# Kernel tuning notes

Measured on AMD Instinct MI355X. Metric: run time of the kernel, lower is better.

The kernel has to match this reference:

```python
import math
import jax, jax.numpy as jnp
import numpy as np

DIM = 256; DEPTH = 5; FANOUT = 10; VOCAB = 257
B = 16; T = 2048
NEXP = 8; HID = 512; TOPK = 2; TEMP = 1.0; HEADS = 2
CAPACITY = math.ceil(B * TOPK / NEXP * 1.1)  # capacity-based dispatch, =5
LAYER_SIZES = [FANOUT ** l for l in range(DEPTH)]  # [1,10,100,1000,10000]


def setup_inputs() -> dict:
    key = jax.random.key(0)
    ks = iter(jax.random.split(key, 64))
    def p(shape, scale=0.02):
        return jax.random.normal(next(ks), shape, jnp.float32) * scale
    inp = {
        'tokens': jax.random.randint(next(ks), (B, T), 0, VOCAB),
        'embed': p((VOCAB, DIM)),
        'pin_w': p((DIM, DIM)), 'pin_b': jnp.zeros(DIM, jnp.float32),
        'pch_w': p((DIM, DIM)), 'pch_b': jnp.zeros(DIM, jnp.float32),
        'depth_bias': p((DEPTH, DIM)),
        'q_w': p((DIM, DIM)), 'q_b': jnp.zeros(DIM, jnp.float32),
        'k_w': p((DIM, DIM)), 'k_b': jnp.zeros(DIM, jnp.float32),
        'v_w': p((DIM, DIM)), 'v_b': jnp.zeros(DIM, jnp.float32),
        'o_w': p((DIM, DIM)), 'o_b': jnp.zeros(DIM, jnp.float32),
        'level_gate': jnp.zeros(DEPTH, jnp.float32),
        'depth_gate': jnp.zeros((DEPTH, DIM), jnp.float32),
        'in_proj_w': p((DIM, 3 * DIM)), 'in_proj_b': jnp.zeros(3 * DIM, jnp.float32),
        'out_proj_w': p((DIM, DIM)), 'out_proj_b': jnp.zeros(DIM, jnp.float32),
        'ln_g': jnp.ones(DIM, jnp.float32), 'ln_b': jnp.zeros(DIM, jnp.float32),
        'ic_gate': jnp.zeros(1, jnp.float32),
        'gate_w': p((DIM, NEXP)), 'gate_b': jnp.zeros(NEXP, jnp.float32),
        'ew1': p((NEXP, DIM, HID)), 'eb1': jnp.zeros((NEXP, HID), jnp.float32),
        'ew2': p((NEXP, HID, DIM)), 'eb2': jnp.zeros((NEXP, DIM), jnp.float32),
        'hw1': p((DIM, DIM)), 'hb1': jnp.zeros(DIM, jnp.float32),
        'hw2': p((DIM, VOCAB)), 'hb2': jnp.zeros(VOCAB, jnp.float32),
    }
    return inp


def _fractal(context, pin_w, pin_b, pch_w, pch_b, depth_bias, q_w, q_b, k_w, k_b,
             v_w, v_b, o_w, o_b, level_gate, depth_gate,
             in_proj_w, in_proj_b, out_proj_w, out_proj_b, ln_g, ln_b, ic_gate):
    Bc = context.shape[0]
    base = context @ pin_w + pin_b                       # [B,D]
    y_next = None
    level_means = [None] * DEPTH
    inv_sqrt_d = 1.0 / math.sqrt(DIM)
    for l in reversed(range(DEPTH)):
        n = LAYER_SIZES[l]
        if l == DEPTH - 1:
            child_agg = jnp.zeros((Bc, n, DIM), context.dtype)
        else:
            yg = y_next.reshape(Bc, n, FANOUT, DIM)      # children grouped per parent
            q = (base + depth_bias[l]) @ q_w + q_b       # [B,D], shared across nodes
            k = yg @ k_w + k_b
            v = yg @ v_w + v_b
            att = jax.nn.softmax(jnp.einsum('bd,bnfd->bnf', q, k) * inv_sqrt_d, axis=-1)
            child_agg = jax.nn.sigmoid(depth_gate[l]) * jnp.einsum('bnf,bnfd->bnd', att, v)
        gate = jax.nn.sigmoid(level_gate[l])
        upd = (base[:, None, :] + depth_bias[l][None, None, :] + child_agg @ pch_w + pch_b) * gate
        y = jax.nn.relu(upd) @ o_w + o_b                 # [B,n,D]
        level_means[l] = y.mean(axis=1)
        y_next = y
    root = y_next[:, 0, :]                               # n==1 at level 0
    # interconnect: MHA over per-level means [B,DEPTH,D]
    z = jnp.stack(level_means, axis=1)
    qkv = z @ in_proj_w + in_proj_b
    qh, kh, vh = jnp.split(qkv, 3, axis=-1)
    hd = DIM // HEADS
    def to_heads(t):
        return t.reshape(Bc, DEPTH, HEADS, hd).transpose(0, 2, 1, 3)
    qh, kh, vh = to_heads(qh), to_heads(kh), to_heads(vh)
    aw = jax.nn.softmax(jnp.einsum('bhqd,bhkd->bhqk', qh, kh) / math.sqrt(hd), axis=-1)
    z2 = jnp.einsum('bhqk,bhkd->bhqd', aw, vh).transpose(0, 2, 1, 3).reshape(Bc, DEPTH, DIM)
    z2 = z2 @ out_proj_w + out_proj_b
    zs = z + z2
    mu = zs.mean(-1, keepdims=True)
    var = ((zs - mu) ** 2).mean(-1, keepdims=True)
    zn = (zs - mu) / jnp.sqrt(var + 1e-5) * ln_g + ln_b
    return root + jax.nn.sigmoid(ic_gate) * zn[:, 0, :]


def _moe(ctx, gate_w, gate_b, ew1, eb1, ew2, eb2):
    scaled = (ctx @ gate_w + gate_b) / TEMP
    top_vals, top_idx = jax.lax.top_k(scaled, TOPK)      # [B,K]
    gs = jax.nn.softmax(top_vals, axis=-1)               # [B,K], strictly > 0
    out = jnp.zeros_like(ctx)
    for e in range(NEXP):                                # fixed small expert loop
        sflat = jnp.where(top_idx == e, gs, -1.0).reshape(-1)   # [B*K]
        vals, pos = jax.lax.top_k(sflat, CAPACITY)       # capacity-limited dispatch
        w = jnp.where(vals > 0.0, vals, 0.0)             # drop unassigned/overflow
        tok = pos // TOPK
        xin = ctx[tok]                                   # [cap,D]
        eo = jax.nn.relu(xin @ ew1[e] + eb1[e]) @ ew2[e] + eb2[e]
        out = out.at[tok].add(eo * w[:, None])
    return out


def reference(tokens, embed, pin_w, pin_b, pch_w, pch_b, depth_bias,
              q_w, q_b, k_w, k_b, v_w, v_b, o_w, o_b, level_gate, depth_gate,
              in_proj_w, in_proj_b, out_proj_w, out_proj_b, ln_g, ln_b, ic_gate,
              gate_w, gate_b, ew1, eb1, ew2, eb2, hw1, hb1, hw2, hb2):
    x = embed[tokens]                                    # [B,T,D]
    context = x.mean(axis=1)                             # [B,D]
    root = _fractal(context, pin_w, pin_b, pch_w, pch_b, depth_bias, q_w, q_b,
                    k_w, k_b, v_w, v_b, o_w, o_b, level_gate, depth_gate,
                    in_proj_w, in_proj_b, out_proj_w, out_proj_b, ln_g, ln_b, ic_gate)
    root = root + _moe(root, gate_w, gate_b, ew1, eb1, ew2, eb2)
    h = x + root[:, None, :]                             # per-token logits from context + token emb
    logits = jax.nn.relu(h @ hw1 + hb1) @ hw2 + hb2      # [B,T,V]
    return logits
```

## Files before the change

kernel.cpp:

```cpp
#include <hip/hip_runtime.h>
#include <hip/hip_bf16.h>
#include <math.h>

#define DIM    256
#define DEPTH  5
#define FANOUT 10
#define VOCAB  257
#define BB     16
#define TT     2048
#define NEXP   8
#define HID    512
#define TOPK   2
#define CAP    5
#define TSTR   260

__device__ __forceinline__ float sigm(float x) { return 1.f / (1.f + expf(-x)); }

__device__ __forceinline__ void mv8x2(const float* sv, const float* __restrict__ W,
                                      int kseg, int cq, float red[16][DIM]) {
  const float* Wp = W + (size_t)kseg * 16 * DIM + cq * 4;
  float4 acc = {0.f, 0.f, 0.f, 0.f};
#pragma unroll 1
  for (int h = 0; h < 2; ++h) {
    float4 wv[8];
#pragma unroll
    for (int i = 0; i < 8; ++i)
      wv[i] = *(const float4*)(Wp + (size_t)(h * 8 + i) * DIM);
#pragma unroll
    for (int i = 0; i < 8; ++i) {
      float s = sv[kseg * 16 + h * 8 + i];
      acc.x = fmaf(s, wv[i].x, acc.x);
      acc.y = fmaf(s, wv[i].y, acc.y);
      acc.z = fmaf(s, wv[i].z, acc.z);
      acc.w = fmaf(s, wv[i].w, acc.w);
    }
    __builtin_amdgcn_sched_barrier(0);
  }
  *(float4*)&red[kseg][cq * 4] = acc;
}

__device__ __forceinline__ float sum16(const float red[16][DIM], int d) {
  float s = 0.f;
#pragma unroll
  for (int g = 0; g < 16; ++g) s += red[g][d];
  return s;
}

__global__ void __launch_bounds__(1024) k_fractal(
    const int* __restrict__ tokens, const float* __restrict__ embed,
    const float* __restrict__ pin_w, const float* __restrict__ pin_b,
    const float* __restrict__ pch_w, const float* __restrict__ pch_b,
    const float* __restrict__ depth_bias,
    const float* __restrict__ v_w, const float* __restrict__ v_b,
    const float* __restrict__ o_w, const float* __restrict__ o_b,
    const float* __restrict__ level_gate, const float* __restrict__ depth_gate,
    const float* __restrict__ in_proj_w, const float* __restrict__ in_proj_b,
    const float* __restrict__ out_proj_w, const float* __restrict__ out_proj_b,
    const float* __restrict__ ln_g, const float* __restrict__ ln_b,
    const float* __restrict__ ic_gate,
    float* __restrict__ rootA) {
  int b = blockIdx.x;
  int tid = threadIdx.x;
  int d = tid & 255;
  int ks = tid >> 8;
  int k0 = ks * 64;
  int kseg = tid >> 6;
  int cq = tid & 63;
  __shared__ int cnt[VOCAB];
  __shared__ float sv[DIM];
  __shared__ float basev[DIM];
  __shared__ float ym[DEPTH][DIM];
  __shared__ float q0v[DIM], kh[DEPTH][DIM], vh[DEPTH][DIM];
  __shared__ float red11[4][11][DIM];
  __shared__ float zsv[DIM];
  __shared__ float aw[16];
  __shared__ float redl[8];
  float (*red16)[DIM] = reinterpret_cast<float(*)[DIM]>(&red11[0][0][0]);

  for (int i = tid; i < VOCAB; i += 1024) cnt[i] = 0;
  __syncthreads();
  for (int t = tid; t < TT; t += 1024) atomicAdd(&cnt[tokens[b * TT + t]], 1);
  __syncthreads();
  {
    const float* Ep = embed + (size_t)kseg * 16 * DIM + cq * 4;
    float4 acc = {0.f, 0.f, 0.f, 0.f};
#pragma unroll 1
    for (int h = 0; h < 2; ++h) {
      float4 ev[8];
#pragma unroll
      for (int i = 0; i < 8; ++i)
        ev[i] = *(const float4*)(Ep + (size_t)(h * 8 + i) * DIM);
#pragma unroll
      for (int i = 0; i < 8; ++i) {
        float cv = (float)cnt[kseg * 16 + h * 8 + i];
        acc.x = fmaf(cv, ev[i].x, acc.x);
        acc.y = fmaf(cv, ev[i].y, acc.y);
        acc.z = fmaf(cv, ev[i].z, acc.z);
        acc.w = fmaf(cv, ev[i].w, acc.w);
      }
      __builtin_amdgcn_sched_barrier(0);
    }
    *(float4*)&red16[kseg][cq * 4] = acc;
  }
  __syncthreads();
  if (ks == 0) {
    float s = sum16(red16, d);
    s = fmaf((float)cnt[256], embed[(size_t)256 * DIM + d], s);
    sv[d] = s * (1.0f / (float)TT);
  }
  __syncthreads();

  mv8x2(sv, pin_w, kseg, cq, red16);
  __syncthreads();
  if (ks == 0) {
    float base = sum16(red16, d) + pin_b[d];
    basev[d] = base;
    float u = (base + depth_bias[4 * DIM + d] + pch_b[d]) * sigm(level_gate[4]);
    sv[d] = fmaxf(u, 0.f);
  }
  __syncthreads();
  mv8x2(sv, o_w, kseg, cq, red16);
  __syncthreads();
  if (ks == 0) {
    float y = sum16(red16, d) + o_b[d];
    ym[4][d] = y;
    sv[d] = y;
  }
  __syncthreads();
  for (int l = 3; l >= 0; --l) {
    mv8x2(sv, v_w, kseg, cq, red16);
    __syncthreads();
    if (ks == 0) {
      float vv = sum16(red16, d) + v_b[d];
      sv[d] = sigm(depth_gate[l * DIM + d]) * vv;
    }
    __syncthreads();
    mv8x2(sv, pch_w, kseg, cq, red16);
    __syncthreads();
    if (ks == 0) {
      float t = sum16(red16, d) + pch_b[d];
      float u = (basev[d] + depth_bias[l * DIM + d] + t) * sigm(level_gate[l]);
      sv[d] = fmaxf(u, 0.f);
    }
    __syncthreads();
    mv8x2(sv, o_w, kseg, cq, red16);
    __syncthreads();
    if (ks == 0) {
      float y = sum16(red16, d) + o_b[d];
      ym[l][d] = y;
      sv[d] = y;
    }
    __syncthreads();
  }
  {
    float aq = 0.f;
    float ak0 = 0.f, ak1 = 0.f, ak2 = 0.f, ak3 = 0.f, ak4 = 0.f;
    float av0 = 0.f, av1 = 0.f, av2 = 0.f, av3 = 0.f, av4 = 0.f;
#pragma unroll
    for (int h = 0; h < 8; ++h) {
      int kb = k0 + h * 8;
      float wq[8], wk[8], wv8[8];
#pragma unroll
      for (int i = 0; i < 8; ++i) {
        const float* wrow = in_proj_w + (size_t)(kb + i) * 768;
        wq[i] = wrow[d]; wk[i] = wrow[256 + d]; wv8[i] = wrow[512 + d];
      }
#pragma unroll
      for (int i = 0; i < 8; ++i) {
        float z0 = ym[0][kb + i];
        aq  = fmaf(z0, wq[i], aq);
        ak0 = fmaf(z0, wk[i], ak0);
        av0 = fmaf(z0, wv8[i], av0);
        float z1 = ym[1][kb + i];
        ak1 = fmaf(z1, wk[i], ak1);
        av1 = fmaf(z1, wv8[i], av1);
        float z2 = ym[2][kb + i];
        ak2 = fmaf(z2, wk[i], ak2);
        av2 = fmaf(z2, wv8[i], av2);
        float z3 = ym[3][kb + i];
        ak3 = fmaf(z3, wk[i], ak3);
        av3 = fmaf(z3, wv8[i], av3);
        float z4 = ym[4][kb + i];
        ak4 = fmaf(z4, wk[i], ak4);
        av4 = fmaf(z4, wv8[i], av4);
      }
    }
    red11[ks][0][d] = ak0; red11[ks][1][d] = ak1; red11[ks][2][d] = ak2;
    red11[ks][3][d] = ak3; red11[ks][4][d] = ak4;
    red11[ks][5][d] = av0; red11[ks][6][d] = av1; red11[ks][7][d] = av2;
    red11[ks][8][d] = av3; red11[ks][9][d] = av4;
    red11[ks][10][d] = aq;
  }
  __syncthreads();
  for (int idx = tid; idx < 11 * DIM; idx += 1024) {
    int c = idx >> 8, dd = idx & 255;
    float sum = red11[0][c][dd] + red11[1][c][dd] + red11[2][c][dd] + red11[3][c][dd];
    if (c < 5)       kh[c][dd]     = sum + in_proj_b[256 + dd];
    else if (c < 10) vh[c - 5][dd] = sum + in_proj_b[512 + dd];
    else             q0v[dd]       = sum + in_proj_b[dd];
  }
  __syncthreads();
  {
    int wid = tid >> 6;
    if (wid < 10) {
      int h = wid / 5, l = wid - h * 5;
      int lane = tid & 63;
      float s = q0v[h * 128 + lane] * kh[l][h * 128 + lane];
      s = fmaf(q0v[h * 128 + 64 + lane], kh[l][h * 128 + 64 + lane], s);
      for (int o = 32; o > 0; o >>= 1) s += __shfl_down(s, o, 64);
      if (lane == 0) aw[wid] = s * 0.08838834764831845f;
    }
  }
  __syncthreads();
  if (tid < 2) {
    float m = aw[tid * 5];
    for (int l = 1; l < 5; ++l) m = fmaxf(m, aw[tid * 5 + l]);
    float e[5], ssum = 0.f;
    for (int l = 0; l < 5; ++l) { e[l] = expf(aw[tid * 5 + l] - m); ssum += e[l]; }
    for (int l = 0; l < 5; ++l) aw[tid * 5 + l] = e[l] / ssum;
  }
  __syncthreads();
  if (ks == 0) {
    int h = d >> 7;
    float z2 = 0.f;
    for (int l = 0; l < 5; ++l) z2 = fmaf(aw[h * 5 + l], vh[l][d], z2);
    sv[d] = z2;
  }
  __syncthreads();
  mv8x2(sv, out_proj_w, kseg, cq, red16);
  __syncthreads();
  if (ks == 0) {
    float z2p = sum16(red16, d) + out_proj_b[d];
    zsv[d] = ym[0][d] + z2p;
  }
  __syncthreads();
  float zs = 0.f, df = 0.f, mu = 0.f;
  if (tid < 256) {
    zs = zsv[tid];
    float v = zs;
    for (int o = 32; o > 0; o >>= 1) v += __shfl_down(v, o, 64);
    if ((tid & 63) == 0) redl[tid >> 6] = v;
  }
  __syncthreads();
  if (tid < 256) {
    mu = (redl[0] + redl[1] + redl[2] + redl[3]) * (1.f / 256.f);
    df = zs - mu;
  }
  __syncthreads();
  if (tid < 256) {
    float v = df * df;
    for (int o = 32; o > 0; o >>= 1) v += __shfl_down(v, o, 64);
    if ((tid & 63) == 0) redl[tid >> 6] = v;
  }
  __syncthreads();
  if (tid < 256) {
    float var = (redl[0] + redl[1] + redl[2] + redl[3]) * (1.f / 256.f);
    float zn = df / sqrtf(var + 1e-5f) * ln_g[tid] + ln_b[tid];
    rootA[b * DIM + tid] = ym[0][tid] + sigm(ic_gate[0]) * zn;
  }
}

__global__ void __launch_bounds__(1024) k_gate(const float* __restrict__ rootA,
                                               const float* __restrict__ gate_w,
                                               const float* __restrict__ gate_b,
                                               int* __restrict__ etok,
                                               float* __restrict__ ewt,
                                               float* __restrict__ root2) {
  __shared__ float red[BB * NEXP][9];
  __shared__ float sc[BB * NEXP];
  __shared__ float gs[BB * TOPK];
  __shared__ int gidx[BB * TOPK];
  int tid = threadIdx.x;
  int be = tid >> 3, ks = tid & 7;
  int b = be >> 3, e = be & 7;
  {
    float acc = 0.f;
#pragma unroll 8
    for (int i = 0; i < 32; ++i) {
      int k = ks * 32 + i;
      acc = fmaf(rootA[b * DIM + k], gate_w[k * NEXP + e], acc);
    }
    red[be][ks] = acc;
  }
  for (int i = tid; i < BB * DIM; i += 1024) root2[i] = rootA[i];
  __syncthreads();
  if (tid < BB * NEXP) {
    float s = gate_b[tid & 7];
#pragma unroll
    for (int g = 0; g < 8; ++g) s += red[tid][g];
    sc[tid] = s;
  }
  __syncthreads();
  if (tid < BB) {
    int bb = tid;
    int i0 = 0; float v0 = sc[bb * 8 + 0];
    for (int ee = 1; ee < 8; ++ee) { float v = sc[bb * 8 + ee]; if (v > v0) { v0 = v; i0 = ee; } }
    int i1 = -1; float v1 = -1e30f;
    for (int ee = 0; ee < 8; ++ee) {
      if (ee == i0) continue;
      float v = sc[bb * 8 + ee];
      if (v > v1) { v1 = v; i1 = ee; }
    }
    float e1 = expf(v1 - v0);
    float s = 1.f + e1;
    gs[bb * 2 + 0] = 1.f / s;  gidx[bb * 2 + 0] = i0;
    gs[bb * 2 + 1] = e1 / s;   gidx[bb * 2 + 1] = i1;
  }
  __syncthreads();
  if (tid < NEXP) {
    int ee = tid;
    unsigned used = 0u;
    for (int s = 0; s < CAP; ++s) {
      int bi = 0; float bv = -1e30f;
      for (int i = 0; i < 32; ++i) {
        if (used & (1u << i)) continue;
        float v = (gidx[i] == ee) ? gs[i] : -1.0f;
        if (v > bv) { bv = v; bi = i; }
      }
      used |= (1u << bi);
      etok[ee * CAP + s] = bi >> 1;
      ewt[ee * CAP + s] = bv > 0.f ? bv : 0.f;
    }
  }
}

__global__ void __launch_bounds__(256) k_expert1(
    const float* __restrict__ rootA,
    const float* __restrict__ ew1, const float* __restrict__ eb1,
    const int* __restrict__ etok,
    float* __restrict__ hid_ws) {
  int bx = blockIdx.x;
  int e = bx >> 3, jt = bx & 7, j0 = jt * 64;
  int tid = threadIdx.x, w = tid >> 6, lane = tid & 63;
  __shared__ float xin[CAP][DIM];
  __shared__ float red[CAP][4][64];
  __shared__ int stok[CAP];
  if (tid < CAP) stok[tid] = etok[e * CAP + tid];
  __syncthreads();
  for (int idx = tid; idx < CAP * DIM; idx += 256) {
    int s = idx >> 8, k = idx & 255;
    xin[s][k] = rootA[stok[s] * DIM + k];
  }
  __syncthreads();
  float a0 = 0.f, a1 = 0.f, a2 = 0.f, a3 = 0.f, a4 = 0.f;
  const float* W = ew1 + (size_t)e * DIM * HID + j0 + lane;
  int kbase = w * 64;
#pragma unroll
  for (int h = 0; h < 8; ++h) {
    float wv[8];
#pragma unroll
    for (int i = 0; i < 8; ++i) wv[i] = W[(size_t)(kbase + h * 8 + i) * HID];
#pragma unroll
    for (int i = 0; i < 8; ++i) {
      int k = kbase + h * 8 + i;
      a0 = fmaf(xin[0][k], wv[i], a0);
      a1 = fmaf(xin[1][k], wv[i], a1);
      a2 = fmaf(xin[2][k], wv[i], a2);
      a3 = fmaf(xin[3][k], wv[i], a3);
      a4 = fmaf(xin[4][k], wv[i], a4);
    }
  }
  red[0][w][lane] = a0; red[1][w][lane] = a1; red[2][w][lane] = a2;
  red[3][w][lane] = a3; red[4][w][lane] = a4;
  __syncthreads();
  for (int idx = tid; idx < CAP * 64; idx += 256) {
    int s = idx >> 6, j = idx & 63;
    float sum = red[s][0][j] + red[s][1][j] + red[s][2][j] + red[s][3][j]
              + eb1[e * HID + j0 + j];
    hid_ws[((size_t)(e * CAP + s)) * HID + j0 + j] = fmaxf(sum, 0.f);
  }
}

__global__ void __launch_bounds__(256) k_expert2(
    const float* __restrict__ hid_ws,
    const float* __restrict__ ew2, const float* __restrict__ eb2,
    const float* __restrict__ ewt, const int* __restrict__ etok,
    float* __restrict__ root2) {
  int bx = blockIdx.x;
  int e = bx >> 3, dt = bx & 7, d0 = dt * 32;
  int tid = threadIdx.x, seg = tid >> 5, c = tid & 31;
  __shared__ float hv[CAP][HID];
  __shared__ float red[CAP][8][32];
  for (int idx = tid; idx < CAP * HID; idx += 256) {
    int s = idx >> 9, k = idx & 511;
    hv[s][k] = hid_ws[((size_t)(e * CAP + s)) * HID + k];
  }
  __syncthreads();
  float a0 = 0.f, a1 = 0.f, a2 = 0.f, a3 = 0.f, a4 = 0.f;
  const float* W = ew2 + (size_t)e * HID * DIM + d0 + c;
  int kbase = seg * 64;
#pragma unroll
  for (int h = 0; h < 8; ++h) {
    float wv[8];
#pragma unroll
    for (int i = 0; i < 8; ++i) wv[i] = W[(size_t)(kbase + h * 8 + i) * DIM];
#pragma unroll
    for (int i = 0; i < 8; ++i) {
      int k = kbase + h * 8 + i;
      a0 = fmaf(hv[0][k], wv[i], a0);
      a1 = fmaf(hv[1][k], wv[i], a1);
      a2 = fmaf(hv[2][k], wv[i], a2);
      a3 = fmaf(hv[3][k], wv[i], a3);
      a4 = fmaf(hv[4][k], wv[i], a4);
    }
  }
  red[0][seg][c] = a0; red[1][seg][c] = a1; red[2][seg][c] = a2;
  red[3][seg][c] = a3; red[4][seg][c] = a4;
  __syncthreads();
  if (tid < CAP * 32) {
    int s = tid >> 5, cc = tid & 31;
    float sum = 0.f;
#pragma unroll
    for (int g = 0; g < 8; ++g) sum += red[s][g][cc];
    sum += eb2[e * DIM + d0 + cc];
    float w = ewt[e * CAP + s];
    if (w > 0.f)
      atomicAdd(&root2[etok[e * CAP + s] * DIM + d0 + cc], sum * w);
  }
}

__global__ void __launch_bounds__(256) k_table(
    const float* __restrict__ embed, const float* __restrict__ root2,
    const float* __restrict__ hw1, const float* __restrict__ hb1,
    const float* __restrict__ hw2, const float* __restrict__ hb2,
    float* __restrict__ table) {
  int tok = blockIdx.x, r0 = blockIdx.y * 4;
  int c = threadIdx.x;
  __shared__ float hrow[4][DIM];
  __shared__ float hid[4][DIM];
  __shared__ float tailred[4][17];
  {
    float ev = embed[(size_t)tok * DIM + c];
#pragma unroll
    for (int j = 0; j < 4; ++j) hrow[j][c] = ev + root2[(size_t)(r0 + j) * DIM + c];
  }
  __syncthreads();
  {
    float a0 = hb1[c], a1 = a0, a2 = a0, a3 = a0;
    for (int kb = 0; kb < DIM; kb += 8) {
      float wv[8];
#pragma unroll
      for (int i = 0; i < 8; ++i) wv[i] = hw1[(size_t)(kb + i) * DIM + c];
#pragma unroll
      for (int i = 0; i < 8; ++i) {
        int k = kb + i;
        a0 = fmaf(hrow[0][k], wv[i], a0);
        a1 = fmaf(hrow[1][k], wv[i], a1);
        a2 = fmaf(hrow[2][k], wv[i], a2);
        a3 = fmaf(hrow[3][k], wv[i], a3);
      }
    }
    hid[0][c] = fmaxf(a0, 0.f); hid[1][c] = fmaxf(a1, 0.f);
    hid[2][c] = fmaxf(a2, 0.f); hid[3][c] = fmaxf(a3, 0.f);
  }
  __syncthreads();
  {
    float a0 = hb2[c], a1 = a0, a2 = a0, a3 = a0;
    for (int kb = 0; kb < DIM; kb += 8) {
      float wv[8];
#pragma unroll
      for (int i = 0; i < 8; ++i) wv[i] = hw2[(size_t)(kb + i) * VOCAB + c];
#pragma unroll
      for (int i = 0; i < 8; ++i) {
        int k = kb + i;
        a0 = fmaf(hid[0][k], wv[i], a0);
        a1 = fmaf(hid[1][k], wv[i], a1);
        a2 = fmaf(hid[2][k], wv[i], a2);
        a3 = fmaf(hid[3][k], wv[i], a3);
      }
    }
    table[((size_t)((r0 + 0) * VOCAB + tok)) * TSTR + c] = a0;
    table[((size_t)((r0 + 1) * VOCAB + tok)) * TSTR + c] = a1;
    table[((size_t)((r0 + 2) * VOCAB + tok)) * TSTR + c] = a2;
    table[((size_t)((r0 + 3) * VOCAB + tok)) * TSTR + c] = a3;
  }
  if (c < 64) {
    int r = c >> 4, seg = c & 15;
    float sum = 0.f;
#pragma unroll 4
    for (int i = 0; i < 16; ++i) {
      int k = seg * 16 + i;
      sum = fmaf(hid[r][k], hw2[(size_t)k * VOCAB + 256], sum);
    }
    tailred[r][seg] = sum;
  }
  __syncthreads();
  if (c < 4) {
    float a = hb2[256];
#pragma unroll
    for (int s = 0; s < 16; ++s) a += tailred[c][s];
    table[((size_t)((r0 + c) * VOCAB + tok)) * TSTR + 256] = a;
  }
}

__global__ void __launch_bounds__(1024) k_scatter(const int* __restrict__ tokens,
                                                  const float* __restrict__ table,
                                                  float* __restrict__ out) {
  int f = blockIdx.x * 1024 + threadIdx.x;
  int row = (int)((unsigned)f / 257u);
  int c = f - row * 257;
  int b = row >> 11;
  int tok = tokens[row];
  out[f] = table[((size_t)(b * VOCAB + tok)) * TSTR + c];
}

extern "C" void kernel_launch(void* const* d_in, const int* in_sizes, int n_in,
                              void* d_out, int out_size, void* d_ws, size_t ws_size,
                              hipStream_t stream) {
  (void)in_sizes; (void)n_in; (void)out_size; (void)ws_size;
  const int*   tokens     = (const int*)d_in[0];
  const float* embed      = (const float*)d_in[1];
  const float* pin_w      = (const float*)d_in[2];
  const float* pin_b      = (const float*)d_in[3];
  const float* pch_w      = (const float*)d_in[4];
  const float* pch_b      = (const float*)d_in[5];
  const float* depth_bias = (const float*)d_in[6];
  const float* v_w        = (const float*)d_in[11];
  const float* v_b        = (const float*)d_in[12];
  const float* o_w        = (const float*)d_in[13];
  const float* o_b        = (const float*)d_in[14];
  const float* level_gate = (const float*)d_in[15];
  const float* depth_gate = (const float*)d_in[16];
  const float* in_proj_w  = (const float*)d_in[17];
  const float* in_proj_b  = (const float*)d_in[18];
  const float* out_proj_w = (const float*)d_in[19];
  const float* out_proj_b = (const float*)d_in[20];
  const float* ln_g       = (const float*)d_in[21];
  const float* ln_b       = (const float*)d_in[22];
  const float* ic_gate    = (const float*)d_in[23];
  const float* gate_w     = (const float*)d_in[24];
  const float* gate_b     = (const float*)d_in[25];
  const float* ew1        = (const float*)d_in[26];
  const float* eb1        = (const float*)d_in[27];
  const float* ew2        = (const float*)d_in[28];
  const float* eb2        = (const float*)d_in[29];
  const float* hw1        = (const float*)d_in[30];
  const float* hb1        = (const float*)d_in[31];
  const float* hw2        = (const float*)d_in[32];
  const float* hb2        = (const float*)d_in[33];
  float* out = (float*)d_out;

  float* ws      = (float*)d_ws;
  float* rootA   = ws + 4096;
  float* root2   = ws + 8192;
  int*   etok    = (int*)(ws + 22528);
  float* ewt     = ws + 22576;
  float* table   = ws + 22656;
  float* hid_ws  = table;

  k_fractal<<<BB, 1024, 0, stream>>>(tokens, embed, pin_w, pin_b, pch_w, pch_b,
                                     depth_bias, v_w, v_b, o_w, o_b, level_gate,
                                     depth_gate, in_proj_w, in_proj_b, out_proj_w,
                                     out_proj_b, ln_g, ln_b, ic_gate, rootA);
  k_gate<<<1, 1024, 0, stream>>>(rootA, gate_w, gate_b, etok, ewt, root2);
  k_expert1<<<NEXP * 8, 256, 0, stream>>>(rootA, ew1, eb1, etok, hid_ws);
  k_expert2<<<NEXP * 8, 256, 0, stream>>>(hid_ws, ew2, eb2, ewt, etok, root2);
  k_table<<<dim3(VOCAB, 4), 256, 0, stream>>>(embed, root2, hw1, hb1, hw2, hb2, table);
  k_scatter<<<(BB * TT * VOCAB) / 1024, 1024, 0, stream>>>(tokens, table, out);
}
```

Before: 264.5 us.

## Fuse gating into expert kernel and scatter logits directly via token buckets

The separate gate kernel is removed: each expert1 block recomputes the gate scores, top-2 selection and capacity assignment redundantly, and root2 is written by the fractal kernel. The fractal kernel also builds per-batch bucket lists of token positions grouped by vocab id. The table kernel then writes each computed logit row straight to every output position holding that token, which eliminates the intermediate table and the separate scatter kernel. Write coalescing now depends on the token distribution, and every expert block repeats the gating work.

Measured after the change: 253.2 us. 1.04x faster.

```diff
diff --git a/kernel.cpp b/kernel.cpp
--- a/kernel.cpp
+++ b/kernel.cpp
@@ -12,7 +12,6 @@
 #define HID    512
 #define TOPK   2
 #define CAP    5
-#define TSTR   260
 
 __device__ __forceinline__ float sigm(float x) { return 1.f / (1.f + expf(-x)); }
 
@@ -58,7 +57,8 @@
     const float* __restrict__ out_proj_w, const float* __restrict__ out_proj_b,
     const float* __restrict__ ln_g, const float* __restrict__ ln_b,
     const float* __restrict__ ic_gate,
-    float* __restrict__ rootA) {
+    float* __restrict__ rootA, float* __restrict__ root2,
+    int* __restrict__ bidx, int* __restrict__ boff) {
   int b = blockIdx.x;
   int tid = threadIdx.x;
   int d = tid & 255;
@@ -75,6 +75,8 @@
   __shared__ float zsv[DIM];
   __shared__ float aw[16];
   __shared__ float redl[8];
+  __shared__ int offb[VOCAB + 1];
+  __shared__ int woff[VOCAB];
   float (*red16)[DIM] = reinterpret_cast<float(*)[DIM]>(&red11[0][0][0]);
 
   for (int i = tid; i < VOCAB; i += 1024) cnt[i] = 0;
@@ -256,38 +258,59 @@
   if (tid < 256) {
     float var = (redl[0] + redl[1] + redl[2] + redl[3]) * (1.f / 256.f);
     float zn = df / sqrtf(var + 1e-5f) * ln_g[tid] + ln_b[tid];
-    rootA[b * DIM + tid] = ym[0][tid] + sigm(ic_gate[0]) * zn;
-  }
-}
-
-__global__ void __launch_bounds__(1024) k_gate(const float* __restrict__ rootA,
-                                               const float* __restrict__ gate_w,
-                                               const float* __restrict__ gate_b,
-                                               int* __restrict__ etok,
-                                               float* __restrict__ ewt,
-                                               float* __restrict__ root2) {
-  __shared__ float red[BB * NEXP][9];
+    float r = ym[0][tid] + sigm(ic_gate[0]) * zn;
+    rootA[b * DIM + tid] = r;
+    root2[b * DIM + tid] = r;
+  }
+  __syncthreads();
+  if (tid == 0) {
+    int a = 0;
+    for (int v = 0; v < VOCAB; ++v) { offb[v] = a; a += cnt[v]; }
+    offb[VOCAB] = a;
+  }
+  __syncthreads();
+  if (tid <= VOCAB) boff[b * (VOCAB + 1) + tid] = offb[tid];
+  if (tid < VOCAB) woff[tid] = offb[tid];
+  __syncthreads();
+  for (int t = tid; t < TT; t += 1024) {
+    int tok = tokens[b * TT + t];
+    int p = atomicAdd(&woff[tok], 1);
+    bidx[b * TT + p] = t;
+  }
+}
+
+__global__ void __launch_bounds__(256) k_expert1(
+    const float* __restrict__ rootA,
+    const float* __restrict__ gate_w, const float* __restrict__ gate_b,
+    const float* __restrict__ ew1, const float* __restrict__ eb1,
+    int* __restrict__ etok, float* __restrict__ ewt,
+    float* __restrict__ hid_ws) {
+  int bx = blockIdx.x;
+  int e = bx >> 3, jt = bx & 7, j0 = jt * 64;
+  int tid = threadIdx.x, w = tid >> 6, lane = tid & 63;
+  __shared__ float xin[CAP][DIM];
+  __shared__ float red[CAP][4][64];
   __shared__ float sc[BB * NEXP];
   __shared__ float gs[BB * TOPK];
   __shared__ int gidx[BB * TOPK];
-  int tid = threadIdx.x;
-  int be = tid >> 3, ks = tid & 7;
-  int b = be >> 3, e = be & 7;
-  {
-    float acc = 0.f;
+  __shared__ int stok[CAP];
+  __shared__ float swt[CAP];
+  if (tid < BB * NEXP) {
+    int b = tid >> 3, ep = tid & 7;
+    float chunk[8];
+#pragma unroll
+    for (int g = 0; g < 8; ++g) {
+      float acc = 0.f;
 #pragma unroll 8
-    for (int i = 0; i < 32; ++i) {
-      int k = ks * 32 + i;
-      acc = fmaf(rootA[b * DIM + k], gate_w[k * NEXP + e], acc);
-    }
-    red[be][ks] = acc;
-  }
-  for (int i = tid; i < BB * DIM; i += 1024) root2[i] = rootA[i];
-  __syncthreads();
-  if (tid < BB * NEXP) {
-    float s = gate_b[tid & 7];
-#pragma unroll
-    for (int g = 0; g < 8; ++g) s += red[tid][g];
+      for (int i = 0; i < 32; ++i) {
+        int k = g * 32 + i;
+        acc = fmaf(rootA[b * DIM + k], gate_w[k * NEXP + ep], acc);
+      }
+      chunk[g] = acc;
+    }
+    float s = gate_b[ep];
+#pragma unroll
+    for (int g = 0; g < 8; ++g) s += chunk[g];
     sc[tid] = s;
   }
   __syncthreads();
@@ -301,42 +324,31 @@
       float v = sc[bb * 8 + ee];
       if (v > v1) { v1 = v; i1 = ee; }
     }
-    float e1 = expf(v1 - v0);
-    float s = 1.f + e1;
+    float e1v = expf(v1 - v0);
+    float s = 1.f + e1v;
     gs[bb * 2 + 0] = 1.f / s;  gidx[bb * 2 + 0] = i0;
-    gs[bb * 2 + 1] = e1 / s;   gidx[bb * 2 + 1] = i1;
-  }
-  __syncthreads();
-  if (tid < NEXP) {
-    int ee = tid;
+    gs[bb * 2 + 1] = e1v / s;  gidx[bb * 2 + 1] = i1;
+  }
+  __syncthreads();
+  if (tid == 0) {
     unsigned used = 0u;
     for (int s = 0; s < CAP; ++s) {
       int bi = 0; float bv = -1e30f;
       for (int i = 0; i < 32; ++i) {
         if (used & (1u << i)) continue;
-        float v = (gidx[i] == ee) ? gs[i] : -1.0f;
+        float v = (gidx[i] == e) ? gs[i] : -1.0f;
         if (v > bv) { bv = v; bi = i; }
       }
       used |= (1u << bi);
-      etok[ee * CAP + s] = bi >> 1;
-      ewt[ee * CAP + s] = bv > 0.f ? bv : 0.f;
-    }
-  }
-}
-
-__global__ void __launch_bounds__(256) k_expert1(
-    const float* __restrict__ rootA,
-    const float* __restrict__ ew1, const float* __restrict__ eb1,
-    const int* __restrict__ etok,
-    float* __restrict__ hid_ws) {
-  int bx = blockIdx.x;
-  int e = bx >> 3, jt = bx & 7, j0 = jt * 64;
-  int tid = threadIdx.x, w = tid >> 6, lane = tid & 63;
-  __shared__ float xin[CAP][DIM];
-  __shared__ float red[CAP][4][64];
-  __shared__ int stok[CAP];
-  if (tid < CAP) stok[tid] = etok[e * CAP + tid];
-  __syncthreads();
+      stok[s] = bi >> 1;
+      swt[s] = bv > 0.f ? bv : 0.f;
+    }
+  }
+  __syncthreads();
+  if (jt == 0 && tid < CAP) {
+    etok[e * CAP + tid] = stok[tid];
+    ewt[e * CAP + tid] = swt[tid];
+  }
   for (int idx = tid; idx < CAP * DIM; idx += 256) {
     int s = idx >> 8, k = idx & 255;
     xin[s][k] = rootA[stok[s] * DIM + k];
@@ -419,16 +431,18 @@
   }
 }
 
-__global__ void __launch_bounds__(256) k_table(
+__global__ void __launch_bounds__(256) k_logits(
     const float* __restrict__ embed, const float* __restrict__ root2,
     const float* __restrict__ hw1, const float* __restrict__ hb1,
     const float* __restrict__ hw2, const float* __restrict__ hb2,
-    float* __restrict__ table) {
+    const int* __restrict__ bidx, const int* __restrict__ boff,
+    float* __restrict__ out) {
   int tok = blockIdx.x, r0 = blockIdx.y * 4;
   int c = threadIdx.x;
   __shared__ float hrow[4][DIM];
   __shared__ float hid[4][DIM];
   __shared__ float tailred[4][17];
+  __shared__ float tailv[4];
   {
     float ev = embed[(size_t)tok * DIM + c];
 #pragma unroll
@@ -454,8 +468,9 @@
     hid[2][c] = fmaxf(a2, 0.f); hid[3][c] = fmaxf(a3, 0.f);
   }
   __syncthreads();
+  float a0, a1, a2, a3;
   {
-    float a0 = hb2[c], a1 = a0, a2 = a0, a3 = a0;
+    a0 = hb2[c]; a1 = a0; a2 = a0; a3 = a0;
     for (int kb = 0; kb < DIM; kb += 8) {
       float wv[8];
 #pragma unroll
@@ -469,10 +484,6 @@
         a3 = fmaf(hid[3][k], wv[i], a3);
       }
     }
-    table[((size_t)((r0 + 0) * VOCAB + tok)) * TSTR + c] = a0;
-    table[((size_t)((r0 + 1) * VOCAB + tok)) * TSTR + c] = a1;
-    table[((size_t)((r0 + 2) * VOCAB + tok)) * TSTR + c] = a2;
-    table[((size_t)((r0 + 3) * VOCAB + tok)) * TSTR + c] = a3;
   }
   if (c < 64) {
     int r = c >> 4, seg = c & 15;
@@ -489,19 +500,23 @@
     float a = hb2[256];
 #pragma unroll
     for (int s = 0; s < 16; ++s) a += tailred[c][s];
-    table[((size_t)((r0 + c) * VOCAB + tok)) * TSTR + 256] = a;
-  }
-}
-
-__global__ void __launch_bounds__(1024) k_scatter(const int* __restrict__ tokens,
-                                                  const float* __restrict__ table,
-                                                  float* __restrict__ out) {
-  int f = blockIdx.x * 1024 + threadIdx.x;
-  int row = (int)((unsigned)f / 257u);
-  int c = f - row * 257;
-  int b = row >> 11;
-  int tok = tokens[row];
-  out[f] = table[((size_t)(b * VOCAB + tok)) * TSTR + c];
+    tailv[c] = a;
+  }
+  __syncthreads();
+#pragma unroll
+  for (int j = 0; j < 4; ++j) {
+    int b = r0 + j;
+    int s = boff[b * (VOCAB + 1) + tok];
+    int e = boff[b * (VOCAB + 1) + tok + 1];
+    float aj = (j == 0) ? a0 : (j == 1) ? a1 : (j == 2) ? a2 : a3;
+    float tl = tailv[j];
+    for (int m = s; m < e; ++m) {
+      int t = bidx[b * TT + m];
+      size_t base = (size_t)(b * TT + t) * VOCAB;
+      out[base + c] = aj;
+      if (c == 0) out[base + 256] = tl;
+    }
+  }
 }
 
 extern "C" void kernel_launch(void* const* d_in, const int* in_sizes, int n_in,
@@ -545,16 +560,18 @@
   float* root2   = ws + 8192;
   int*   etok    = (int*)(ws + 22528);
   float* ewt     = ws + 22576;
-  float* table   = ws + 22656;
-  float* hid_ws  = table;
+  float* hid_ws  = ws + 22656;
+  int*   bidx    = (int*)(ws + 43136);
+  int*   boff    = (int*)(ws + 75904);
 
   k_fractal<<<BB, 1024, 0, stream>>>(tokens, embed, pin_w, pin_b, pch_w, pch_b,
                                      depth_bias, v_w, v_b, o_w, o_b, level_gate,
                                      depth_gate, in_proj_w, in_proj_b, out_proj_w,
-                                     out_proj_b, ln_g, ln_b, ic_gate, rootA);
-  k_gate<<<1, 1024, 0, stream>>>(rootA, gate_w, gate_b, etok, ewt, root2);
-  k_expert1<<<NEXP * 8, 256, 0, stream>>>(rootA, ew1, eb1, etok, hid_ws);
+                                     out_proj_b, ln_g, ln_b, ic_gate, rootA, root2,
+                                     bidx, boff);
+  k_expert1<<<NEXP * 8, 256, 0, stream>>>(rootA, gate_w, gate_b, ew1, eb1,
+                                          etok, ewt, hid_ws);
   k_expert2<<<NEXP * 8, 256, 0, stream>>>(hid_ws, ew2, eb2, ewt, etok, root2);
-  k_table<<<dim3(VOCAB, 4), 256, 0, stream>>>(embed, root2, hw1, hb1, hw2, hb2, table);
-  k_scatter<<<(BB * TT * VOCAB) / 1024, 1024, 0, stream>>>(tokens, table, out);
-}
+  k_logits<<<dim3(VOCAB, 4), 256, 0, stream>>>(embed, root2, hw1, hb1, hw2, hb2,
+                                               bidx, boff, out);
+}
```
